# Optimization experiments

Hardware: AMD Instinct MI355X
Metric: run time of the kernel (lower is better)

## Reference

```python
import jax, jax.numpy as jnp
import numpy as np

USER_VOCAB = 2_000_000
ITEM_VOCAB = 1_000_000
EMB = 64
TOWER = [128, 64]
BATCH = 524_288


def _mlp_params(key, dims):
    params = []
    prev = EMB
    for d in dims:
        key, k1, k2 = jax.random.split(key, 3)
        bound = 1.0 / np.sqrt(prev)
        W = jax.random.uniform(k1, (prev, d), jnp.float32, -bound, bound)
        b = jax.random.uniform(k2, (d,), jnp.float32, -bound, bound)
        params.extend([W, b])
        prev = d
    return params


def setup_inputs() -> dict:
    key = jax.random.key(0)
    ks = jax.random.split(key, 6)
    user_ids = jax.random.randint(ks[0], (BATCH,), 0, USER_VOCAB, dtype=jnp.int64 if jax.config.jax_enable_x64 else jnp.int32)
    item_ids = jax.random.randint(ks[1], (BATCH,), 0, ITEM_VOCAB, dtype=jnp.int64 if jax.config.jax_enable_x64 else jnp.int32)
    user_table = jax.random.normal(ks[2], (USER_VOCAB, EMB), jnp.float32) * 0.02
    item_table = jax.random.normal(ks[3], (ITEM_VOCAB, EMB), jnp.float32) * 0.02
    uW1, ub1, uW2, ub2 = _mlp_params(ks[4], TOWER)
    iW1, ib1, iW2, ib2 = _mlp_params(ks[5], TOWER)
    return {
        "user_ids": user_ids, "item_ids": item_ids,
        "user_table": user_table, "item_table": item_table,
        "uW1": uW1, "ub1": ub1, "uW2": uW2, "ub2": ub2,
        "iW1": iW1, "ib1": ib1, "iW2": iW2, "ib2": ib2,
    }


def _tower(x, W1, b1, W2, b2):
    h = jax.nn.relu(x @ W1 + b1)
    return jax.nn.relu(h @ W2 + b2)


def _l2norm(x, eps=1e-12):
    # matches F.normalize(p=2): x / max(||x||, eps)
    n = jnp.sqrt(jnp.sum(x * x, axis=-1, keepdims=True))
    return x / jnp.maximum(n, eps)


def reference(user_ids, item_ids, user_table, item_table,
              uW1, ub1, uW2, ub2, iW1, ib1, iW2, ib2):
    user_emb = user_table[user_ids]          # [B, EMB] irregular gather
    item_emb = item_table[item_ids]          # [B, EMB]
    user_vec = _l2norm(_tower(user_emb, uW1, ub1, uW2, ub2))
    item_vec = _l2norm(_tower(item_emb, iW1, ib1, iW2, ib2))
    return jnp.sum(user_vec * item_vec, axis=-1)  # [B]
```

## Files before the change

kernel.cpp:

```cpp
#include <hip/hip_runtime.h>
#include <math.h>
#include <stdint.h>

typedef _Float16 f16;
typedef _Float16 f16x8 __attribute__((ext_vector_type(8)));
typedef float f32x16 __attribute__((ext_vector_type(16)));

#define WS_UW1T 0
#define WS_UW2T 18432
#define WS_IW1T 35840
#define WS_IW2T 54272
#define WS_BIAS 71680

__global__ __launch_bounds__(256) void prep_kernel(
    const float* __restrict__ uW1, const float* __restrict__ ub1,
    const float* __restrict__ uW2, const float* __restrict__ ub2,
    const float* __restrict__ iW1, const float* __restrict__ ib1,
    const float* __restrict__ iW2, const float* __restrict__ ib2,
    char* __restrict__ ws)
{
  int g = blockIdx.x * 256 + threadIdx.x;
  if (g < 8192) {
    int n = g >> 6, k = g & 63;
    ((f16*)(ws + WS_UW1T))[n * 72 + k] = (f16)uW1[k * 128 + n];
  } else if (g < 16384) {
    int j = g - 8192; int n = j >> 7, k = j & 127;
    ((f16*)(ws + WS_UW2T))[n * 136 + k] = (f16)uW2[k * 64 + n];
  } else if (g < 24576) {
    int j = g - 16384; int n = j >> 6, k = j & 63;
    ((f16*)(ws + WS_IW1T))[n * 72 + k] = (f16)iW1[k * 128 + n];
  } else if (g < 32768) {
    int j = g - 24576; int n = j >> 7, k = j & 127;
    ((f16*)(ws + WS_IW2T))[n * 136 + k] = (f16)iW2[k * 64 + n];
  } else if (g < 33152) {
    int j = g - 32768;
    float v = (j < 128) ? ub1[j]
            : (j < 192) ? ub2[j - 128]
            : (j < 320) ? ib1[j - 192]
                        : ib2[j - 320];
    ((float*)(ws + WS_BIAS))[j] = v;
  }
}

__device__ inline f32x16 zero16() {
  f32x16 z;
#pragma unroll
  for (int i = 0; i < 16; ++i) z[i] = 0.f;
  return z;
}

__device__ inline void copy16(const char* __restrict__ g, char* s, int nbytes, int tid) {
  const uint4* gs = (const uint4*)g;
  uint4* ss = (uint4*)s;
  int n = nbytes >> 4;
  for (int j = tid; j < n; j += 256) ss[j] = gs[j];
}

__device__ inline void stage_x(const int* __restrict__ ids, const float* __restrict__ table,
                               f16* sX, int base, int tid) {
  int row = tid >> 1, half = tid & 1;
  int id = ids[base + row];
  const float4* src = (const float4*)(table + (size_t)id * 64 + half * 32);
  f16* dst = sX + row * 72 + half * 32;
#pragma unroll
  for (int j = 0; j < 4; ++j) {
    float4 v0 = src[2 * j], v1 = src[2 * j + 1];
    f16x8 p;
    p[0] = (f16)v0.x; p[1] = (f16)v0.y; p[2] = (f16)v0.z; p[3] = (f16)v0.w;
    p[4] = (f16)v1.x; p[5] = (f16)v1.y; p[6] = (f16)v1.z; p[7] = (f16)v1.w;
    *(f16x8*)(dst + j * 8) = p;
  }
}

__device__ inline void run_tower(
    const f16* sX, f16* sW, f16* sH, const float* sB,
    const char* __restrict__ ws_w2t,
    int bias1_off, int bias2_off,
    int tid, int wave, int l31, int lhi,
    f32x16& out0, f32x16& out1)
{
  const int mt0 = (wave >> 1) * 2, nt0 = (wave & 1) * 2;
  f32x16 h00 = zero16(), h01 = zero16(), h10 = zero16(), h11 = zero16();
#pragma unroll
  for (int ks = 0; ks < 4; ++ks) {
    int ko = ks * 16 + lhi * 8;
    f16x8 a0 = *(const f16x8*)(sX + (mt0 * 32 + l31) * 72 + ko);
    f16x8 a1 = *(const f16x8*)(sX + (mt0 * 32 + 32 + l31) * 72 + ko);
    f16x8 b0 = *(const f16x8*)(sW + (nt0 * 32 + l31) * 72 + ko);
    f16x8 b1 = *(const f16x8*)(sW + (nt0 * 32 + 32 + l31) * 72 + ko);
    h00 = __builtin_amdgcn_mfma_f32_32x32x16_f16(a0, b0, h00, 0, 0, 0);
    h01 = __builtin_amdgcn_mfma_f32_32x32x16_f16(a0, b1, h01, 0, 0, 0);
    h10 = __builtin_amdgcn_mfma_f32_32x32x16_f16(a1, b0, h10, 0, 0, 0);
    h11 = __builtin_amdgcn_mfma_f32_32x32x16_f16(a1, b1, h11, 0, 0, 0);
  }
  {
    float bias0 = sB[bias1_off + nt0 * 32 + l31];
    float bias1 = sB[bias1_off + nt0 * 32 + 32 + l31];
    int col0 = nt0 * 32 + l31, col1 = col0 + 32;
#pragma unroll
    for (int r = 0; r < 16; ++r) {
      int rophys = (r & 3) + 8 * (r >> 2) + 4 * lhi;
      int row0 = mt0 * 32 + rophys, row1 = row0 + 32;
      sH[row0 * 136 + col0] = (f16)fmaxf(h00[r] + bias0, 0.f);
      sH[row0 * 136 + col1] = (f16)fmaxf(h01[r] + bias1, 0.f);
      sH[row1 * 136 + col0] = (f16)fmaxf(h10[r] + bias0, 0.f);
      sH[row1 * 136 + col1] = (f16)fmaxf(h11[r] + bias1, 0.f);
    }
  }
  __syncthreads();
  copy16(ws_w2t, (char*)sW, 17408, tid);
  __syncthreads();

  const int mt = wave;
  f32x16 v0 = zero16(), v1 = zero16();
#pragma unroll
  for (int ks = 0; ks < 8; ++ks) {
    int ko = ks * 16 + lhi * 8;
    f16x8 a  = *(const f16x8*)(sH + (mt * 32 + l31) * 136 + ko);
    f16x8 b0 = *(const f16x8*)(sW + (l31) * 136 + ko);
    f16x8 b1 = *(const f16x8*)(sW + (32 + l31) * 136 + ko);
    v0 = __builtin_amdgcn_mfma_f32_32x32x16_f16(a, b0, v0, 0, 0, 0);
    v1 = __builtin_amdgcn_mfma_f32_32x32x16_f16(a, b1, v1, 0, 0, 0);
  }
  float b20 = sB[bias2_off + l31], b21 = sB[bias2_off + 32 + l31];
#pragma unroll
  for (int r = 0; r < 16; ++r) {
    out0[r] = fmaxf(v0[r] + b20, 0.f);
    out1[r] = fmaxf(v1[r] + b21, 0.f);
  }
}

__global__ __launch_bounds__(256, 2) void TwoTowerModel_71708773974789_kernel(
    const int* __restrict__ user_ids, const int* __restrict__ item_ids,
    const float* __restrict__ user_table, const float* __restrict__ item_table,
    const char* __restrict__ ws, float* __restrict__ out)
{
  __shared__ __attribute__((aligned(16))) char smem[73216];
  f16* sX = (f16*)smem;
  f16* sW = (f16*)(smem + 18432);
  f16* sH = (f16*)(smem + 36864);
  float* sB = (float*)(smem + 71680);

  const int tid = threadIdx.x;
  const int wave = tid >> 6, lane = tid & 63, l31 = lane & 31, lhi = lane >> 5;
  const int rbase = blockIdx.x * 128;

  copy16(ws + WS_UW1T, (char*)sW, 18432, tid);
  for (int j = tid; j < 384; j += 256) sB[j] = ((const float*)(ws + WS_BIAS))[j];
  stage_x(user_ids, user_table, sX, rbase, tid);
  __syncthreads();

  f32x16 u0, u1, i0, i1;
  run_tower(sX, sW, sH, sB, ws + WS_UW2T, 0, 128, tid, wave, l31, lhi, u0, u1);
  __syncthreads();

  copy16(ws + WS_IW1T, (char*)sW, 18432, tid);
  stage_x(item_ids, item_table, sX, rbase, tid);
  __syncthreads();

  run_tower(sX, sW, sH, sB, ws + WS_IW2T, 192, 320, tid, wave, l31, lhi, i0, i1);
  __syncthreads();

#pragma unroll
  for (int r = 0; r < 16; ++r) {
    int row = wave * 32 + (r & 3) + 8 * (r >> 2) + 4 * lhi;
    sX[row * 72 + l31]      = (f16)u0[r];
    sX[row * 72 + 32 + l31] = (f16)u1[r];
    sW[row * 72 + l31]      = (f16)i0[r];
    sW[row * 72 + 32 + l31] = (f16)i1[r];
  }
  __syncthreads();

  {
    int row = tid >> 1, half = tid & 1;
    const f16x8* up = (const f16x8*)(sX + row * 72 + half * 32);
    const f16x8* ip = (const f16x8*)(sW + row * 72 + half * 32);
    float sui = 0.f, suu = 0.f, sii = 0.f;
#pragma unroll
    for (int j = 0; j < 4; ++j) {
      f16x8 uv = up[j], iv = ip[j];
#pragma unroll
      for (int e = 0; e < 8; ++e) {
        float uf = (float)uv[e], vf = (float)iv[e];
        sui += uf * vf; suu += uf * uf; sii += vf * vf;
      }
    }
    sui += __shfl_xor(sui, 1);
    suu += __shfl_xor(suu, 1);
    sii += __shfl_xor(sii, 1);
    if (half == 0) {
      float nu = fmaxf(sqrtf(suu), 1e-12f);
      float nv = fmaxf(sqrtf(sii), 1e-12f);
      out[rbase + row] = sui / (nu * nv);
    }
  }
}

extern "C" void kernel_launch(void* const* d_in, const int* in_sizes, int n_in,
                              void* d_out, int out_size, void* d_ws, size_t ws_size,
                              hipStream_t stream) {
  const int*   user_ids   = (const int*)d_in[0];
  const int*   item_ids   = (const int*)d_in[1];
  const float* user_table = (const float*)d_in[2];
  const float* item_table = (const float*)d_in[3];
  const float* uW1 = (const float*)d_in[4];
  const float* ub1 = (const float*)d_in[5];
  const float* uW2 = (const float*)d_in[6];
  const float* ub2 = (const float*)d_in[7];
  const float* iW1 = (const float*)d_in[8];
  const float* ib1 = (const float*)d_in[9];
  const float* iW2 = (const float*)d_in[10];
  const float* ib2 = (const float*)d_in[11];
  char* ws = (char*)d_ws;

  prep_kernel<<<130, 256, 0, stream>>>(uW1, ub1, uW2, ub2, iW1, ib1, iW2, ib2, ws);
  int nblk = out_size / 128;
  TwoTowerModel_71708773974789_kernel<<<nblk, 256, 0, stream>>>(
      user_ids, item_ids, user_table, item_table, ws, (float*)d_out);
}
```

Baseline: 774.2 us.

## Halve block tile, read weights from global, issue both gathers up front

Each block now handles 64 rows instead of 128, and the MLP weight and bias matrices are read directly from global/L2 rather than staged into LDS. This cuts shared memory from about 73KB to 35KB and raises the launch-bounds occupancy target from 2 to 4 blocks. Both the user and item embedding gathers are issued at kernel start into registers, so the item gather latency overlaps the user tower compute. The cost is repeated global weight reads per wave, which depend on cache hits, plus higher register pressure from holding the item rows.

```diff
diff --git a/kernel.cpp b/kernel.cpp
--- a/kernel.cpp
+++ b/kernel.cpp
@@ -49,146 +49,129 @@
   return z;
 }
 
-__device__ inline void copy16(const char* __restrict__ g, char* s, int nbytes, int tid) {
-  const uint4* gs = (const uint4*)g;
-  uint4* ss = (uint4*)s;
-  int n = nbytes >> 4;
-  for (int j = tid; j < n; j += 256) ss[j] = gs[j];
-}
-
-__device__ inline void stage_x(const int* __restrict__ ids, const float* __restrict__ table,
-                               f16* sX, int base, int tid) {
-  int row = tid >> 1, half = tid & 1;
-  int id = ids[base + row];
-  const float4* src = (const float4*)(table + (size_t)id * 64 + half * 32);
-  f16* dst = sX + row * 72 + half * 32;
-#pragma unroll
-  for (int j = 0; j < 4; ++j) {
-    float4 v0 = src[2 * j], v1 = src[2 * j + 1];
-    f16x8 p;
-    p[0] = (f16)v0.x; p[1] = (f16)v0.y; p[2] = (f16)v0.z; p[3] = (f16)v0.w;
-    p[4] = (f16)v1.x; p[5] = (f16)v1.y; p[6] = (f16)v1.z; p[7] = (f16)v1.w;
-    *(f16x8*)(dst + j * 8) = p;
-  }
-}
-
-__device__ inline void run_tower(
-    const f16* sX, f16* sW, f16* sH, const float* sB,
-    const char* __restrict__ ws_w2t,
-    int bias1_off, int bias2_off,
-    int tid, int wave, int l31, int lhi,
-    f32x16& out0, f32x16& out1)
+__device__ inline f16x8 pack8(float4 a, float4 b) {
+  f16x8 p;
+  p[0] = (f16)a.x; p[1] = (f16)a.y; p[2] = (f16)a.z; p[3] = (f16)a.w;
+  p[4] = (f16)b.x; p[5] = (f16)b.y; p[6] = (f16)b.z; p[7] = (f16)b.w;
+  return p;
+}
+
+__device__ inline void tower(
+    const f16* __restrict__ sX, f16* __restrict__ sH,
+    const f16* __restrict__ gW1t, const f16* __restrict__ gW2t,
+    const float* __restrict__ gB1, const float* __restrict__ gB2,
+    int wave, int l31, int lhi, f32x16& u)
 {
-  const int mt0 = (wave >> 1) * 2, nt0 = (wave & 1) * 2;
-  f32x16 h00 = zero16(), h01 = zero16(), h10 = zero16(), h11 = zero16();
+  const int mt = wave >> 1, ntb = (wave & 1) * 2;
+  f32x16 h0 = zero16(), h1 = zero16();
 #pragma unroll
   for (int ks = 0; ks < 4; ++ks) {
     int ko = ks * 16 + lhi * 8;
-    f16x8 a0 = *(const f16x8*)(sX + (mt0 * 32 + l31) * 72 + ko);
-    f16x8 a1 = *(const f16x8*)(sX + (mt0 * 32 + 32 + l31) * 72 + ko);
-    f16x8 b0 = *(const f16x8*)(sW + (nt0 * 32 + l31) * 72 + ko);
-    f16x8 b1 = *(const f16x8*)(sW + (nt0 * 32 + 32 + l31) * 72 + ko);
-    h00 = __builtin_amdgcn_mfma_f32_32x32x16_f16(a0, b0, h00, 0, 0, 0);
-    h01 = __builtin_amdgcn_mfma_f32_32x32x16_f16(a0, b1, h01, 0, 0, 0);
-    h10 = __builtin_amdgcn_mfma_f32_32x32x16_f16(a1, b0, h10, 0, 0, 0);
-    h11 = __builtin_amdgcn_mfma_f32_32x32x16_f16(a1, b1, h11, 0, 0, 0);
-  }
-  {
-    float bias0 = sB[bias1_off + nt0 * 32 + l31];
-    float bias1 = sB[bias1_off + nt0 * 32 + 32 + l31];
-    int col0 = nt0 * 32 + l31, col1 = col0 + 32;
+    f16x8 a  = *(const f16x8*)(sX + (mt * 32 + l31) * 72 + ko);
+    f16x8 b0 = *(const f16x8*)(gW1t + (ntb * 32 + l31) * 72 + ko);
+    f16x8 b1 = *(const f16x8*)(gW1t + (ntb * 32 + 32 + l31) * 72 + ko);
+    h0 = __builtin_amdgcn_mfma_f32_32x32x16_f16(a, b0, h0, 0, 0, 0);
+    h1 = __builtin_amdgcn_mfma_f32_32x32x16_f16(a, b1, h1, 0, 0, 0);
+  }
+  {
+    float bias0 = gB1[ntb * 32 + l31];
+    float bias1 = gB1[ntb * 32 + 32 + l31];
+    int col0 = ntb * 32 + l31, col1 = col0 + 32;
 #pragma unroll
     for (int r = 0; r < 16; ++r) {
-      int rophys = (r & 3) + 8 * (r >> 2) + 4 * lhi;
-      int row0 = mt0 * 32 + rophys, row1 = row0 + 32;
-      sH[row0 * 136 + col0] = (f16)fmaxf(h00[r] + bias0, 0.f);
-      sH[row0 * 136 + col1] = (f16)fmaxf(h01[r] + bias1, 0.f);
-      sH[row1 * 136 + col0] = (f16)fmaxf(h10[r] + bias0, 0.f);
-      sH[row1 * 136 + col1] = (f16)fmaxf(h11[r] + bias1, 0.f);
-    }
-  }
-  __syncthreads();
-  copy16(ws_w2t, (char*)sW, 17408, tid);
-  __syncthreads();
-
-  const int mt = wave;
-  f32x16 v0 = zero16(), v1 = zero16();
+      int row = mt * 32 + (r & 3) + 8 * (r >> 2) + 4 * lhi;
+      sH[row * 136 + col0] = (f16)fmaxf(h0[r] + bias0, 0.f);
+      sH[row * 136 + col1] = (f16)fmaxf(h1[r] + bias1, 0.f);
+    }
+  }
+  __syncthreads();
+
+  const int nt = wave & 1;
+  f32x16 v = zero16();
 #pragma unroll
   for (int ks = 0; ks < 8; ++ks) {
     int ko = ks * 16 + lhi * 8;
-    f16x8 a  = *(const f16x8*)(sH + (mt * 32 + l31) * 136 + ko);
-    f16x8 b0 = *(const f16x8*)(sW + (l31) * 136 + ko);
-    f16x8 b1 = *(const f16x8*)(sW + (32 + l31) * 136 + ko);
-    v0 = __builtin_amdgcn_mfma_f32_32x32x16_f16(a, b0, v0, 0, 0, 0);
-    v1 = __builtin_amdgcn_mfma_f32_32x32x16_f16(a, b1, v1, 0, 0, 0);
-  }
-  float b20 = sB[bias2_off + l31], b21 = sB[bias2_off + 32 + l31];
-#pragma unroll
-  for (int r = 0; r < 16; ++r) {
-    out0[r] = fmaxf(v0[r] + b20, 0.f);
-    out1[r] = fmaxf(v1[r] + b21, 0.f);
-  }
-}
-
-__global__ __launch_bounds__(256, 2) void TwoTowerModel_71708773974789_kernel(
+    f16x8 a = *(const f16x8*)(sH + (mt * 32 + l31) * 136 + ko);
+    f16x8 b = *(const f16x8*)(gW2t + (nt * 32 + l31) * 136 + ko);
+    v = __builtin_amdgcn_mfma_f32_32x32x16_f16(a, b, v, 0, 0, 0);
+  }
+  float b2 = gB2[nt * 32 + l31];
+#pragma unroll
+  for (int r = 0; r < 16; ++r) u[r] = fmaxf(v[r] + b2, 0.f);
+}
+
+__global__ __launch_bounds__(256, 4) void TwoTowerModel_71708773974789_kernel(
     const int* __restrict__ user_ids, const int* __restrict__ item_ids,
     const float* __restrict__ user_table, const float* __restrict__ item_table,
     const char* __restrict__ ws, float* __restrict__ out)
 {
-  __shared__ __attribute__((aligned(16))) char smem[73216];
+  __shared__ __attribute__((aligned(16))) char smem[35840];
   f16* sX = (f16*)smem;
-  f16* sW = (f16*)(smem + 18432);
-  f16* sH = (f16*)(smem + 36864);
-  float* sB = (float*)(smem + 71680);
+  f16* sH = (f16*)(smem + 9216);
+  f16* sI = (f16*)(smem + 26624);
+
+  const f16*   gUW1 = (const f16*)(ws + WS_UW1T);
+  const f16*   gUW2 = (const f16*)(ws + WS_UW2T);
+  const f16*   gIW1 = (const f16*)(ws + WS_IW1T);
+  const f16*   gIW2 = (const f16*)(ws + WS_IW2T);
+  const float* gB   = (const float*)(ws + WS_BIAS);
 
   const int tid = threadIdx.x;
   const int wave = tid >> 6, lane = tid & 63, l31 = lane & 31, lhi = lane >> 5;
-  const int rbase = blockIdx.x * 128;
-
-  copy16(ws + WS_UW1T, (char*)sW, 18432, tid);
-  for (int j = tid; j < 384; j += 256) sB[j] = ((const float*)(ws + WS_BIAS))[j];
-  stage_x(user_ids, user_table, sX, rbase, tid);
-  __syncthreads();
-
-  f32x16 u0, u1, i0, i1;
-  run_tower(sX, sW, sH, sB, ws + WS_UW2T, 0, 128, tid, wave, l31, lhi, u0, u1);
-  __syncthreads();
-
-  copy16(ws + WS_IW1T, (char*)sW, 18432, tid);
-  stage_x(item_ids, item_table, sX, rbase, tid);
-  __syncthreads();
-
-  run_tower(sX, sW, sH, sB, ws + WS_IW2T, 192, 320, tid, wave, l31, lhi, i0, i1);
-  __syncthreads();
-
-#pragma unroll
-  for (int r = 0; r < 16; ++r) {
-    int row = wave * 32 + (r & 3) + 8 * (r >> 2) + 4 * lhi;
-    sX[row * 72 + l31]      = (f16)u0[r];
-    sX[row * 72 + 32 + l31] = (f16)u1[r];
-    sW[row * 72 + l31]      = (f16)i0[r];
-    sW[row * 72 + 32 + l31] = (f16)i1[r];
-  }
-  __syncthreads();
-
-  {
-    int row = tid >> 1, half = tid & 1;
-    const f16x8* up = (const f16x8*)(sX + row * 72 + half * 32);
-    const f16x8* ip = (const f16x8*)(sW + row * 72 + half * 32);
+  const int rbase = blockIdx.x * 64;
+  const int row = tid >> 2, q = tid & 3;
+
+  const int uid = user_ids[rbase + row];
+  const int iid = item_ids[rbase + row];
+  const float4* usrc = (const float4*)(user_table + (size_t)uid * 64 + q * 16);
+  const float4* isrc = (const float4*)(item_table + (size_t)iid * 64 + q * 16);
+  float4 ua = usrc[0], ub = usrc[1], uc = usrc[2], ud = usrc[3];
+  float4 pa = isrc[0], pb = isrc[1], pc = isrc[2], pd = isrc[3];
+
+  {
+    f16x8* dst = (f16x8*)(sX + row * 72 + q * 16);
+    dst[0] = pack8(ua, ub);
+    dst[1] = pack8(uc, ud);
+  }
+  __syncthreads();
+
+  f32x16 u, iacc;
+  tower(sX, sH, gUW1, gUW2, gB + 0, gB + 128, wave, l31, lhi, u);
+  {
+    f16x8* dst = (f16x8*)(sX + row * 72 + q * 16);
+    dst[0] = pack8(pa, pb);
+    dst[1] = pack8(pc, pd);
+  }
+  __syncthreads();
+
+  tower(sX, sH, gIW1, gIW2, gB + 192, gB + 320, wave, l31, lhi, iacc);
+  {
+    const int mt = wave >> 1, nt = wave & 1;
+#pragma unroll
+    for (int r = 0; r < 16; ++r) {
+      int rr = mt * 32 + (r & 3) + 8 * (r >> 2) + 4 * lhi;
+      sX[rr * 72 + nt * 32 + l31] = (f16)u[r];
+      sI[rr * 72 + nt * 32 + l31] = (f16)iacc[r];
+    }
+  }
+  __syncthreads();
+
+  {
+    const f16x8* up = (const f16x8*)(sX + row * 72 + q * 16);
+    const f16x8* ip = (const f16x8*)(sI + row * 72 + q * 16);
+    f16x8 u0 = up[0], u1 = up[1], i0 = ip[0], i1 = ip[1];
     float sui = 0.f, suu = 0.f, sii = 0.f;
 #pragma unroll
-    for (int j = 0; j < 4; ++j) {
-      f16x8 uv = up[j], iv = ip[j];
-#pragma unroll
-      for (int e = 0; e < 8; ++e) {
-        float uf = (float)uv[e], vf = (float)iv[e];
-        sui += uf * vf; suu += uf * uf; sii += vf * vf;
-      }
-    }
-    sui += __shfl_xor(sui, 1);
-    suu += __shfl_xor(suu, 1);
-    sii += __shfl_xor(sii, 1);
-    if (half == 0) {
+    for (int e = 0; e < 8; ++e) {
+      float a0 = (float)u0[e], b0 = (float)i0[e];
+      float a1 = (float)u1[e], b1 = (float)i1[e];
+      sui += a0 * b0 + a1 * b1;
+      suu += a0 * a0 + a1 * a1;
+      sii += b0 * b0 + b1 * b1;
+    }
+    sui += __shfl_xor(sui, 1); suu += __shfl_xor(suu, 1); sii += __shfl_xor(sii, 1);
+    sui += __shfl_xor(sui, 2); suu += __shfl_xor(suu, 2); sii += __shfl_xor(sii, 2);
+    if (q == 0) {
       float nu = fmaxf(sqrtf(suu), 1e-12f);
       float nv = fmaxf(sqrtf(sii), 1e-12f);
       out[rbase + row] = sui / (nu * nv);
@@ -214,7 +197,7 @@
   char* ws = (char*)d_ws;
 
   prep_kernel<<<130, 256, 0, stream>>>(uW1, ub1, uW2, ub2, iW1, ib1, iW2, ib2, ws);
-  int nblk = out_size / 128;
+  int nblk = out_size / 64;
   TwoTowerModel_71708773974789_kernel<<<nblk, 256, 0, stream>>>(
       user_ids, item_ids, user_table, item_table, ws, (float*)d_out);
 }
```

After: 776.4 us. Within noise of the previous version (+0.3%).
